# Kernel optimization log

Hardware: AMD Instinct MI355X
Metric: run time of the kernel (lower is better)

Reference implementation:

```python
import jax, jax.numpy as jnp
import numpy as np

WIN = 64
SHIFT = 32
HEADS = 12


def setup_inputs() -> dict:
    key = jax.random.key(0)
    ks = jax.random.split(key, 6)
    D = 768
    return {
        'x': jax.random.normal(ks[0], (16, 4096, D), dtype=jnp.float32),
        'qkv_w': jax.random.normal(ks[1], (3 * D, D), dtype=jnp.float32) * (D ** -0.5),
        'qkv_b': jax.random.normal(ks[2], (3 * D,), dtype=jnp.float32) * 0.02,
        'proj_w': jax.random.normal(ks[3], (D, D), dtype=jnp.float32) * (D ** -0.5),
        'proj_b': jax.random.normal(ks[4], (D,), dtype=jnp.float32) * 0.02,
        'rel_bias': jax.random.normal(ks[5], (HEADS, 2 * WIN - 1), dtype=jnp.float32) * 0.02,
    }


def reference(x, qkv_w, qkv_b, proj_w, proj_b, rel_bias):
    B, N, D = x.shape
    H, hd = HEADS, D // HEADS
    scale = hd ** -0.5
    if SHIFT:
        x = jnp.roll(x, SHIFT, axis=1)
    pad = (-N) % WIN
    if pad:
        x = jnp.pad(x, ((0, 0), (0, pad), (0, 0)))
    Np = x.shape[1]
    nW = Np // WIN
    # [B*nW, w, D] windows
    xw = x.reshape(B * nW, WIN, D)
    qkv = xw @ qkv_w.T + qkv_b                       # [B*nW, w, 3D]
    qkv = qkv.reshape(B * nW, WIN, 3, H, hd).transpose(2, 0, 3, 1, 4)
    q, k, v = qkv[0], qkv[1], qkv[2]                 # [B*nW, H, w, hd]
    attn = jnp.einsum('bhqd,bhkd->bhqk', q, k) * scale
    idx = jnp.arange(WIN)
    rel = idx[None, :] - idx[:, None] + (WIN - 1)    # [w, w] in [0, 2w-2]
    attn = attn + rel_bias[:, rel][None]             # gather bias per head
    attn = jax.nn.softmax(attn, axis=-1)
    y = jnp.einsum('bhqk,bhkd->bhqd', attn, v)       # [B*nW, H, w, hd]
    y = y.transpose(0, 2, 1, 3).reshape(B * nW, WIN, D)
    y = y @ proj_w.T + proj_b
    y = y.reshape(B, Np, D)
    if pad:
        y = y[:, :N, :]
    if SHIFT:
        y = jnp.roll(y, -SHIFT, axis=1)
    return y
```

## Files before the change

### kernel.cpp

```cpp
#include <hip/hip_runtime.h>
#include <hip/hip_bf16.h>
#include <stdint.h>

#define SEQ     4096
#define NBATCH  16
#define DMODEL  768
#define NHEAD   12
#define HDIM    64
#define WINSZ   64
#define SHIFT_T 32
#define QKV_N   (3*DMODEL)

typedef __attribute__((ext_vector_type(8))) short  bf16x8;
typedef __attribute__((ext_vector_type(4))) float  f32x4;

static __device__ __forceinline__ unsigned short f2bf(float f) {
  union { float f; unsigned u; } v; v.f = f;
  unsigned r = v.u + 0x7fffu + ((v.u >> 16) & 1u);
  return (unsigned short)(r >> 16);
}

#define G2L(gp, lp) __builtin_amdgcn_global_load_lds( \
    (const __attribute__((address_space(1))) unsigned*)(const void*)(gp), \
    (__attribute__((address_space(3))) unsigned*)(void*)(lp), 16, 0, 0)

__global__ void k_cvt_x(const float* __restrict__ x, unsigned short* __restrict__ xb,
                        long long c0, long long n8) {
  for (long long i = (long long)blockIdx.x*blockDim.x + threadIdx.x; i < n8;
       i += (long long)gridDim.x*blockDim.x) {
    long long e = i*8;
    int d = (int)(e % DMODEL);
    long long gt = c0 + e / DMODEL;
    int t = (int)(gt & (SEQ-1));
    long long b = gt >> 12;
    int ts = (t - SHIFT_T) & (SEQ-1);
    const float* src = x + (((b << 12) + ts) * (long long)DMODEL + d);
    float4 a0 = *(const float4*)src;
    float4 a1 = *(const float4*)(src + 4);
    bf16x8 o;
    o[0]=(short)f2bf(a0.x); o[1]=(short)f2bf(a0.y); o[2]=(short)f2bf(a0.z); o[3]=(short)f2bf(a0.w);
    o[4]=(short)f2bf(a1.x); o[5]=(short)f2bf(a1.y); o[6]=(short)f2bf(a1.z); o[7]=(short)f2bf(a1.w);
    *(bf16x8*)(xb + e) = o;
  }
}

__global__ void k_cvt_w(const float* __restrict__ w, unsigned short* __restrict__ wb, int n8) {
  int i = blockIdx.x*blockDim.x + threadIdx.x;
  if (i >= n8) return;
  float4 a0 = ((const float4*)w)[2*i];
  float4 a1 = ((const float4*)w)[2*i+1];
  bf16x8 o;
  o[0]=(short)f2bf(a0.x); o[1]=(short)f2bf(a0.y); o[2]=(short)f2bf(a0.z); o[3]=(short)f2bf(a0.w);
  o[4]=(short)f2bf(a1.x); o[5]=(short)f2bf(a1.y); o[6]=(short)f2bf(a1.z); o[7]=(short)f2bf(a1.w);
  ((bf16x8*)wb)[i] = o;
}

template<int MODE>
__global__ __launch_bounds__(512, 1)
void k_gemm256(const unsigned short* __restrict__ A, const unsigned short* __restrict__ Bw,
               const float* __restrict__ bias, unsigned short* __restrict__ Cb,
               float* __restrict__ Cf, int M, int N, int K, int nTN, long long c0) {
  __shared__ char lds[4*32768];
  const int nsl = K >> 5;
  int nwg = gridDim.x;
  int cpx = nwg >> 3;
  int wg  = (blockIdx.x & 7) * cpx + (blockIdx.x >> 3);
  int bm = wg / nTN, bn = wg - bm*nTN;
  long long m0 = (long long)bm * 256;
  int n0 = bn * 256;
  int tid = threadIdx.x;
  int lane = tid & 63, wid = tid >> 6;
  int wr = wid >> 2, wc = wid & 3;
  int cl = lane & 15, g4 = lane >> 4;

  const long long K2 = 2LL * K;
  int L  = tid * 16;
  int Ls = L ^ (((L >> 7) & 7) << 4);
  int srow = Ls >> 6;
  int scol = Ls & 63;
  const char* gA0 = (const char*)A + (m0 + srow) * K2 + scol;
  const char* gA1 = (const char*)A + (m0 + 128 + srow) * K2 + scol;
  const char* gB0 = (const char*)Bw + (long long)(n0 + srow) * K2 + scol;
  const char* gB1 = (const char*)Bw + (long long)(n0 + 128 + srow) * K2 + scol;
  int ldst = L;

  int aoff = (wr*8192 + cl*64 + g4*16) ^ ((cl >> 1) << 4);
  int boff = (16384 + wc*4096 + cl*64 + g4*16) ^ ((cl >> 1) << 4);

  f32x4 acc[8][4];
  #pragma unroll
  for (int i = 0; i < 8; ++i)
    #pragma unroll
    for (int j = 0; j < 4; ++j) acc[i][j] = (f32x4){0.f,0.f,0.f,0.f};

  {
    char* s0 = lds;
    char* s1 = lds + 32768;
    G2L(gA0,       s0 + ldst);
    G2L(gA1,       s0 + 8192  + ldst);
    G2L(gB0,       s0 + 16384 + ldst);
    G2L(gB1,       s0 + 24576 + ldst);
    G2L(gA0 + 64,  s1 + ldst);
    G2L(gA1 + 64,  s1 + 8192  + ldst);
    G2L(gB0 + 64,  s1 + 16384 + ldst);
    G2L(gB1 + 64,  s1 + 24576 + ldst);
    asm volatile("s_waitcnt vmcnt(4)" ::: "memory");
    __builtin_amdgcn_sched_barrier(0);
    __builtin_amdgcn_s_barrier();
  }

#define MFMA_ROW(av, m) \
    acc[m][0] = __builtin_amdgcn_mfma_f32_16x16x32_bf16(av, b0, acc[m][0], 0, 0, 0); \
    acc[m][1] = __builtin_amdgcn_mfma_f32_16x16x32_bf16(av, b1, acc[m][1], 0, 0, 0); \
    acc[m][2] = __builtin_amdgcn_mfma_f32_16x16x32_bf16(av, b2, acc[m][2], 0, 0, 0); \
    acc[m][3] = __builtin_amdgcn_mfma_f32_16x16x32_bf16(av, b3, acc[m][3], 0, 0, 0);

  for (int s = 0; s < nsl; ++s) {
    char* sb  = lds + ((s & 3) << 15);
    char* stb = lds + (((s + 2) & 3) << 15);
    long long kb2 = (long long)(s + 2) << 6;
    bool doStage = (s + 2) < nsl;

    bf16x8 a0 = *(const bf16x8*)(sb + aoff);
    bf16x8 a1 = *(const bf16x8*)(sb + aoff + 1024);
    bf16x8 a2 = *(const bf16x8*)(sb + aoff + 2048);
    bf16x8 a3 = *(const bf16x8*)(sb + aoff + 3072);
    bf16x8 b0 = *(const bf16x8*)(sb + boff);
    bf16x8 b1 = *(const bf16x8*)(sb + boff + 1024);
    bf16x8 b2 = *(const bf16x8*)(sb + boff + 2048);
    bf16x8 b3 = *(const bf16x8*)(sb + boff + 3072);
    if (doStage) {
      G2L(gA0 + kb2, stb + ldst);
      G2L(gA1 + kb2, stb + 8192 + ldst);
    }
    __builtin_amdgcn_sched_barrier(0);
    __builtin_amdgcn_s_barrier();
    asm volatile("s_waitcnt lgkmcnt(0)" ::: "memory");
    __builtin_amdgcn_sched_barrier(0);
    __builtin_amdgcn_s_setprio(1);
    MFMA_ROW(a0, 0)
    MFMA_ROW(a1, 1)
    MFMA_ROW(a2, 2)
    MFMA_ROW(a3, 3)
    __builtin_amdgcn_s_setprio(0);
    __builtin_amdgcn_sched_barrier(0);
    __builtin_amdgcn_s_barrier();

    bf16x8 a4 = *(const bf16x8*)(sb + aoff + 4096);
    bf16x8 a5 = *(const bf16x8*)(sb + aoff + 5120);
    bf16x8 a6 = *(const bf16x8*)(sb + aoff + 6144);
    bf16x8 a7 = *(const bf16x8*)(sb + aoff + 7168);
    if (doStage) {
      G2L(gB0 + kb2, stb + 16384 + ldst);
      G2L(gB1 + kb2, stb + 24576 + ldst);
      asm volatile("s_waitcnt vmcnt(4)" ::: "memory");
    } else if (s + 1 < nsl) {
      asm volatile("s_waitcnt vmcnt(0)" ::: "memory");
    }
    __builtin_amdgcn_sched_barrier(0);
    __builtin_amdgcn_s_barrier();
    asm volatile("s_waitcnt lgkmcnt(0)" ::: "memory");
    __builtin_amdgcn_sched_barrier(0);
    __builtin_amdgcn_s_setprio(1);
    MFMA_ROW(a4, 4)
    MFMA_ROW(a5, 5)
    MFMA_ROW(a6, 6)
    MFMA_ROW(a7, 7)
    __builtin_amdgcn_s_setprio(0);
    __builtin_amdgcn_sched_barrier(0);
    __builtin_amdgcn_s_barrier();
  }
#undef MFMA_ROW

  #pragma unroll
  for (int mf = 0; mf < 8; ++mf) {
    #pragma unroll
    for (int nf = 0; nf < 4; ++nf) {
      int n = n0 + wc*64 + nf*16 + cl;
      float bv = bias[n];
      #pragma unroll
      for (int r = 0; r < 4; ++r) {
        long long m = m0 + wr*128 + mf*16 + g4*4 + r;
        float v = acc[mf][nf][r] + bv;
        if (MODE == 0) {
          Cb[m * (long long)N + n] = f2bf(v);
        } else {
          long long gm = c0 + m;
          long long om = (gm & ~(long long)(SEQ-1)) | ((gm - SHIFT_T) & (long long)(SEQ-1));
          Cf[om * (long long)N + n] = v;
        }
      }
    }
  }
}

__global__ __launch_bounds__(256, 4)
void k_attn(const unsigned short* __restrict__ qkv, const float* __restrict__ rel_bias,
            unsigned short* __restrict__ y) {
  int w = blockIdx.x / NHEAD;
  int h = blockIdx.x - w*NHEAD;
  __shared__ unsigned short sQ[64*72], sK[64*72], sV[64*72];
  __shared__ unsigned short sP[4][16*72];
  __shared__ float rb[128];
  int tid = threadIdx.x, lane = tid & 63, wid = tid >> 6;
  int cl = lane & 15, g4 = lane >> 4;

  if (tid < 2*WINSZ - 1) rb[tid] = rel_bias[h*(2*WINSZ-1) + tid];

  const unsigned short* base = qkv + (long long)w*WINSZ*QKV_N + h*HDIM;
  #pragma unroll
  for (int pass = 0; pass < 2; ++pass) {
    int row = (tid >> 3) + pass*32;
    int ch  = tid & 7;
    const unsigned short* src = base + (long long)row*QKV_N + ch*8;
    *(bf16x8*)(sQ + row*72 + ch*8) = *(const bf16x8*)(src);
    *(bf16x8*)(sK + row*72 + ch*8) = *(const bf16x8*)(src + DMODEL);
    *(bf16x8*)(sV + row*72 + ch*8) = *(const bf16x8*)(src + 2*DMODEL);
  }
  __syncthreads();

  f32x4 sc[4];
  #pragma unroll
  for (int nt = 0; nt < 4; ++nt) sc[nt] = (f32x4){0.f,0.f,0.f,0.f};
  #pragma unroll
  for (int kk = 0; kk < 2; ++kk) {
    bf16x8 aq = *(const bf16x8*)(sQ + (wid*16 + cl)*72 + kk*32 + g4*8);
    #pragma unroll
    for (int nt = 0; nt < 4; ++nt) {
      bf16x8 bk = *(const bf16x8*)(sK + (nt*16 + cl)*72 + kk*32 + g4*8);
      sc[nt] = __builtin_amdgcn_mfma_f32_16x16x32_bf16(aq, bk, sc[nt], 0, 0, 0);
    }
  }

  float pv[4][4];
  #pragma unroll
  for (int r = 0; r < 4; ++r) {
    int qi = wid*16 + g4*4 + r;
    float mx = -1e30f;
    #pragma unroll
    for (int nt = 0; nt < 4; ++nt) {
      int kj = nt*16 + cl;
      float v = sc[nt][r]*0.125f + rb[kj - qi + (WINSZ-1)];
      pv[nt][r] = v;
      mx = fmaxf(mx, v);
    }
    #pragma unroll
    for (int m = 1; m < 16; m <<= 1) mx = fmaxf(mx, __shfl_xor(mx, m, 64));
    float sum = 0.f;
    #pragma unroll
    for (int nt = 0; nt < 4; ++nt) { float e = __expf(pv[nt][r]-mx); pv[nt][r] = e; sum += e; }
    #pragma unroll
    for (int m = 1; m < 16; m <<= 1) sum += __shfl_xor(sum, m, 64);
    float inv = 1.f / sum;
    #pragma unroll
    for (int nt = 0; nt < 4; ++nt)
      sP[wid][(g4*4+r)*72 + nt*16 + cl] = f2bf(pv[nt][r]*inv);
  }

  f32x4 o[4];
  #pragma unroll
  for (int nt = 0; nt < 4; ++nt) o[nt] = (f32x4){0.f,0.f,0.f,0.f};
  #pragma unroll
  for (int kk = 0; kk < 2; ++kk) {
    bf16x8 ap = *(const bf16x8*)(&sP[wid][cl*72 + kk*32 + g4*8]);
    #pragma unroll
    for (int nt = 0; nt < 4; ++nt) {
      bf16x8 bv;
      #pragma unroll
      for (int j = 0; j < 8; ++j)
        bv[j] = (short)sV[(kk*32 + g4*8 + j)*72 + nt*16 + cl];
      o[nt] = __builtin_amdgcn_mfma_f32_16x16x32_bf16(ap, bv, o[nt], 0, 0, 0);
    }
  }

  long long tokbase = (long long)w * WINSZ;
  #pragma unroll
  for (int nt = 0; nt < 4; ++nt)
    #pragma unroll
    for (int r = 0; r < 4; ++r) {
      int row = wid*16 + g4*4 + r;
      y[(tokbase + row) * (long long)DMODEL + h*HDIM + nt*16 + cl] = f2bf(o[nt][r]);
    }
}

extern "C" void kernel_launch(void* const* d_in, const int* in_sizes, int n_in,
                              void* d_out, int out_size, void* d_ws, size_t ws_size,
                              hipStream_t stream) {
  const float* x      = (const float*)d_in[0];
  const float* qkv_w  = (const float*)d_in[1];
  const float* qkv_b  = (const float*)d_in[2];
  const float* proj_w = (const float*)d_in[3];
  const float* proj_b = (const float*)d_in[4];
  const float* rel_b  = (const float*)d_in[5];
  float* out = (float*)d_out;

  const long long NTOK = (long long)NBATCH * SEQ;
  const size_t wbytes = (size_t)QKV_N*DMODEL*2 + (size_t)DMODEL*DMODEL*2;

  int C = 16;
  for (int c : {1, 2, 4, 8, 16}) {
    size_t tpc = (size_t)NTOK / c;
    size_t need = tpc*QKV_N*2 + tpc*DMODEL*2 + wbytes;
    if (need <= ws_size) { C = c; break; }
  }
  long long tpc = NTOK / C;

  char* ws = (char*)d_ws;
  unsigned short* qkvb = (unsigned short*)ws;
  unsigned short* xb   = (unsigned short*)(ws + (size_t)tpc*QKV_N*2);
  unsigned short* wq   = (unsigned short*)(ws + (size_t)tpc*QKV_N*2 + (size_t)tpc*DMODEL*2);
  unsigned short* wp   = wq + (size_t)QKV_N*DMODEL;

  k_cvt_w<<<(QKV_N*DMODEL/8 + 255)/256, 256, 0, stream>>>(qkv_w, wq, QKV_N*DMODEL/8);
  k_cvt_w<<<(DMODEL*DMODEL/8 + 255)/256, 256, 0, stream>>>(proj_w, wp, DMODEL*DMODEL/8);

  for (int c = 0; c < C; ++c) {
    long long c0 = (long long)c * tpc;
    long long n8 = tpc * DMODEL / 8;
    int cvtGrid = (int)((n8 + 255) / 256); if (cvtGrid > 2048) cvtGrid = 2048;
    k_cvt_x<<<cvtGrid, 256, 0, stream>>>(x, xb, c0, n8);

    int mT = (int)(tpc / 256);
    k_gemm256<0><<<mT * (QKV_N/256), 512, 0, stream>>>(xb, wq, qkv_b, qkvb, nullptr,
                                                       (int)tpc, QKV_N, DMODEL, QKV_N/256, c0);
    k_attn<<<(int)(tpc/WINSZ) * NHEAD, 256, 0, stream>>>(qkvb, rel_b, xb );
    k_gemm256<1><<<mT * (DMODEL/256), 512, 0, stream>>>(xb, wp, proj_b, nullptr, out,
                                                        (int)tpc, DMODEL, DMODEL, DMODEL/256, c0);
  }
}
```

Measured before the change: 525.7 us.

## Switch GEMM to 32x32x16 MFMA with single-phase unrolled K pipeline

Replaces the 16x16x32 MFMA tiling in the QKV/projection GEMM with 32x32x16 bf16 MFMAs. Each wave still covers a 128x64 tile, now as 4x2 32x32 blocks that need fewer LDS fragment loads per MFMA. The K loop becomes one phase per slice with both A and B staged together, manually unrolled by four ring slots, with fewer barriers per slice. The epilogue index mapping is updated for the 32x32 accumulator layout. This relies on nsl being at least 4, and on the four-slot ring with vmcnt(4) waits staying correct.

```diff
diff --git a/kernel.cpp b/kernel.cpp
--- a/kernel.cpp
+++ b/kernel.cpp
@@ -11,8 +11,9 @@
 #define SHIFT_T 32
 #define QKV_N   (3*DMODEL)
 
-typedef __attribute__((ext_vector_type(8))) short  bf16x8;
-typedef __attribute__((ext_vector_type(4))) float  f32x4;
+typedef __attribute__((ext_vector_type(8)))  short bf16x8;
+typedef __attribute__((ext_vector_type(4)))  float f32x4;
+typedef __attribute__((ext_vector_type(16))) float f32x16;
 
 static __device__ __forceinline__ unsigned short f2bf(float f) {
   union { float f; unsigned u; } v; v.f = f;
@@ -55,6 +56,8 @@
   ((bf16x8*)wb)[i] = o;
 }
 
+#define MFMA32(a,b,c) __builtin_amdgcn_mfma_f32_32x32x16_bf16(a,b,c,0,0,0)
+
 template<int MODE>
 __global__ __launch_bounds__(512, 1)
 void k_gemm256(const unsigned short* __restrict__ A, const unsigned short* __restrict__ Bw,
@@ -71,117 +74,106 @@
   int tid = threadIdx.x;
   int lane = tid & 63, wid = tid >> 6;
   int wr = wid >> 2, wc = wid & 3;
-  int cl = lane & 15, g4 = lane >> 4;
+  int l31 = lane & 31, h = lane >> 5;
 
   const long long K2 = 2LL * K;
   int L  = tid * 16;
   int Ls = L ^ (((L >> 7) & 7) << 4);
-  int srow = Ls >> 6;
-  int scol = Ls & 63;
+  int srow = Ls >> 6, scol = Ls & 63;
   const char* gA0 = (const char*)A + (m0 + srow) * K2 + scol;
   const char* gA1 = (const char*)A + (m0 + 128 + srow) * K2 + scol;
   const char* gB0 = (const char*)Bw + (long long)(n0 + srow) * K2 + scol;
   const char* gB1 = (const char*)Bw + (long long)(n0 + 128 + srow) * K2 + scol;
-  int ldst = L;
-
-  int aoff = (wr*8192 + cl*64 + g4*16) ^ ((cl >> 1) << 4);
-  int boff = (16384 + wc*4096 + cl*64 + g4*16) ^ ((cl >> 1) << 4);
-
-  f32x4 acc[8][4];
-  #pragma unroll
-  for (int i = 0; i < 8; ++i)
-    #pragma unroll
-    for (int j = 0; j < 4; ++j) acc[i][j] = (f32x4){0.f,0.f,0.f,0.f};
-
-  {
-    char* s0 = lds;
-    char* s1 = lds + 32768;
-    G2L(gA0,       s0 + ldst);
-    G2L(gA1,       s0 + 8192  + ldst);
-    G2L(gB0,       s0 + 16384 + ldst);
-    G2L(gB1,       s0 + 24576 + ldst);
-    G2L(gA0 + 64,  s1 + ldst);
-    G2L(gA1 + 64,  s1 + 8192  + ldst);
-    G2L(gB0 + 64,  s1 + 16384 + ldst);
-    G2L(gB1 + 64,  s1 + 24576 + ldst);
-    asm volatile("s_waitcnt vmcnt(4)" ::: "memory");
-    __builtin_amdgcn_sched_barrier(0);
-    __builtin_amdgcn_s_barrier();
-  }
-
-#define MFMA_ROW(av, m) \
-    acc[m][0] = __builtin_amdgcn_mfma_f32_16x16x32_bf16(av, b0, acc[m][0], 0, 0, 0); \
-    acc[m][1] = __builtin_amdgcn_mfma_f32_16x16x32_bf16(av, b1, acc[m][1], 0, 0, 0); \
-    acc[m][2] = __builtin_amdgcn_mfma_f32_16x16x32_bf16(av, b2, acc[m][2], 0, 0, 0); \
-    acc[m][3] = __builtin_amdgcn_mfma_f32_16x16x32_bf16(av, b3, acc[m][3], 0, 0, 0);
-
-  for (int s = 0; s < nsl; ++s) {
-    char* sb  = lds + ((s & 3) << 15);
-    char* stb = lds + (((s + 2) & 3) << 15);
-    long long kb2 = (long long)(s + 2) << 6;
-    bool doStage = (s + 2) < nsl;
-
-    bf16x8 a0 = *(const bf16x8*)(sb + aoff);
-    bf16x8 a1 = *(const bf16x8*)(sb + aoff + 1024);
-    bf16x8 a2 = *(const bf16x8*)(sb + aoff + 2048);
-    bf16x8 a3 = *(const bf16x8*)(sb + aoff + 3072);
-    bf16x8 b0 = *(const bf16x8*)(sb + boff);
-    bf16x8 b1 = *(const bf16x8*)(sb + boff + 1024);
-    bf16x8 b2 = *(const bf16x8*)(sb + boff + 2048);
-    bf16x8 b3 = *(const bf16x8*)(sb + boff + 3072);
-    if (doStage) {
-      G2L(gA0 + kb2, stb + ldst);
-      G2L(gA1 + kb2, stb + 8192 + ldst);
-    }
-    __builtin_amdgcn_sched_barrier(0);
-    __builtin_amdgcn_s_barrier();
-    asm volatile("s_waitcnt lgkmcnt(0)" ::: "memory");
-    __builtin_amdgcn_sched_barrier(0);
-    __builtin_amdgcn_s_setprio(1);
-    MFMA_ROW(a0, 0)
-    MFMA_ROW(a1, 1)
-    MFMA_ROW(a2, 2)
-    MFMA_ROW(a3, 3)
-    __builtin_amdgcn_s_setprio(0);
-    __builtin_amdgcn_sched_barrier(0);
-    __builtin_amdgcn_s_barrier();
-
-    bf16x8 a4 = *(const bf16x8*)(sb + aoff + 4096);
-    bf16x8 a5 = *(const bf16x8*)(sb + aoff + 5120);
-    bf16x8 a6 = *(const bf16x8*)(sb + aoff + 6144);
-    bf16x8 a7 = *(const bf16x8*)(sb + aoff + 7168);
-    if (doStage) {
-      G2L(gB0 + kb2, stb + 16384 + ldst);
-      G2L(gB1 + kb2, stb + 24576 + ldst);
-      asm volatile("s_waitcnt vmcnt(4)" ::: "memory");
-    } else if (s + 1 < nsl) {
-      asm volatile("s_waitcnt vmcnt(0)" ::: "memory");
-    }
-    __builtin_amdgcn_sched_barrier(0);
-    __builtin_amdgcn_s_barrier();
-    asm volatile("s_waitcnt lgkmcnt(0)" ::: "memory");
-    __builtin_amdgcn_sched_barrier(0);
-    __builtin_amdgcn_s_setprio(1);
-    MFMA_ROW(a4, 4)
-    MFMA_ROW(a5, 5)
-    MFMA_ROW(a6, 6)
-    MFMA_ROW(a7, 7)
-    __builtin_amdgcn_s_setprio(0);
-    __builtin_amdgcn_sched_barrier(0);
-    __builtin_amdgcn_s_barrier();
-  }
-#undef MFMA_ROW
-
-  #pragma unroll
-  for (int mf = 0; mf < 8; ++mf) {
-    #pragma unroll
-    for (int nf = 0; nf < 4; ++nf) {
-      int n = n0 + wc*64 + nf*16 + cl;
+
+  int axor  = ((l31 >> 1) & 7) << 4;
+  int aoff0 = wr*8192 + ((l31*64 + h*16) ^ axor);
+  int aoff1 = aoff0 ^ 32;
+  int boff0 = 16384 + (wc >> 1)*8192 + ((((wc & 1)*64 + l31)*64 + h*16) ^ axor);
+  int boff1 = boff0 ^ 32;
+
+  f32x16 acc[4][2];
+  #pragma unroll
+  for (int i = 0; i < 4; ++i)
+    #pragma unroll
+    for (int j = 0; j < 2; ++j)
+      #pragma unroll
+      for (int e = 0; e < 16; ++e) acc[i][j][e] = 0.f;
+
+  G2L(gA0,      lds + L);
+  G2L(gA1,      lds + 8192  + L);
+  G2L(gB0,      lds + 16384 + L);
+  G2L(gB1,      lds + 24576 + L);
+  G2L(gA0 + 64, lds + 32768 + L);
+  G2L(gA1 + 64, lds + 32768 + 8192  + L);
+  G2L(gB0 + 64, lds + 32768 + 16384 + L);
+  G2L(gB1 + 64, lds + 32768 + 24576 + L);
+  gA0 += 128; gA1 += 128; gB0 += 128; gB1 += 128;
+  asm volatile("s_waitcnt vmcnt(4)" ::: "memory");
+  __builtin_amdgcn_sched_barrier(0);
+  __builtin_amdgcn_s_barrier();
+
+#define SLICE(SLOT, STSLOT, DO_STAGE, VMASM) do {                          \
+    const char* sb = lds + (SLOT)*32768;                                   \
+    bf16x8 a0 = *(const bf16x8*)(sb + aoff0);                              \
+    bf16x8 a1 = *(const bf16x8*)(sb + aoff0 + 2048);                       \
+    bf16x8 a2 = *(const bf16x8*)(sb + aoff0 + 4096);                       \
+    bf16x8 a3 = *(const bf16x8*)(sb + aoff0 + 6144);                       \
+    bf16x8 a4 = *(const bf16x8*)(sb + aoff1);                              \
+    bf16x8 a5 = *(const bf16x8*)(sb + aoff1 + 2048);                       \
+    bf16x8 a6 = *(const bf16x8*)(sb + aoff1 + 4096);                       \
+    bf16x8 a7 = *(const bf16x8*)(sb + aoff1 + 6144);                       \
+    bf16x8 b0 = *(const bf16x8*)(sb + boff0);                              \
+    bf16x8 b1 = *(const bf16x8*)(sb + boff0 + 2048);                       \
+    bf16x8 b2 = *(const bf16x8*)(sb + boff1);                              \
+    bf16x8 b3 = *(const bf16x8*)(sb + boff1 + 2048);                       \
+    if (DO_STAGE) {                                                        \
+      char* st = lds + (STSLOT)*32768;                                     \
+      G2L(gA0, st + L);                                                    \
+      G2L(gA1, st + 8192  + L);                                            \
+      G2L(gB0, st + 16384 + L);                                            \
+      G2L(gB1, st + 24576 + L);                                            \
+    }                                                                      \
+    gA0 += 64; gA1 += 64; gB0 += 64; gB1 += 64;                            \
+    asm volatile(VMASM ::: "memory");                                      \
+    __builtin_amdgcn_sched_barrier(0);                                     \
+    __builtin_amdgcn_s_barrier();                                          \
+    __builtin_amdgcn_s_setprio(1);                                         \
+    acc[0][0]=MFMA32(a0,b0,acc[0][0]); acc[0][1]=MFMA32(a0,b1,acc[0][1]);  \
+    acc[1][0]=MFMA32(a1,b0,acc[1][0]); acc[1][1]=MFMA32(a1,b1,acc[1][1]);  \
+    acc[2][0]=MFMA32(a2,b0,acc[2][0]); acc[2][1]=MFMA32(a2,b1,acc[2][1]);  \
+    acc[3][0]=MFMA32(a3,b0,acc[3][0]); acc[3][1]=MFMA32(a3,b1,acc[3][1]);  \
+    acc[0][0]=MFMA32(a4,b2,acc[0][0]); acc[0][1]=MFMA32(a4,b3,acc[0][1]);  \
+    acc[1][0]=MFMA32(a5,b2,acc[1][0]); acc[1][1]=MFMA32(a5,b3,acc[1][1]);  \
+    acc[2][0]=MFMA32(a6,b2,acc[2][0]); acc[2][1]=MFMA32(a6,b3,acc[2][1]);  \
+    acc[3][0]=MFMA32(a7,b2,acc[3][0]); acc[3][1]=MFMA32(a7,b3,acc[3][1]);  \
+    __builtin_amdgcn_s_setprio(0);                                         \
+    __builtin_amdgcn_sched_barrier(0);                                     \
+    __builtin_amdgcn_s_barrier();                                          \
+  } while (0)
+
+  for (int os = 0; os + 8 <= nsl; os += 4) {
+    SLICE(0, 2, true, "s_waitcnt vmcnt(4)");
+    SLICE(1, 3, true, "s_waitcnt vmcnt(4)");
+    SLICE(2, 0, true, "s_waitcnt vmcnt(4)");
+    SLICE(3, 1, true, "s_waitcnt vmcnt(4)");
+  }
+  SLICE(0, 2, true,  "s_waitcnt vmcnt(4)");
+  SLICE(1, 3, true,  "s_waitcnt vmcnt(4)");
+  SLICE(2, 0, false, "s_waitcnt vmcnt(0)");
+  SLICE(3, 1, false, "");
+#undef SLICE
+
+  #pragma unroll
+  for (int mt = 0; mt < 4; ++mt) {
+    #pragma unroll
+    for (int nt = 0; nt < 2; ++nt) {
+      int n = n0 + wc*64 + nt*32 + l31;
       float bv = bias[n];
       #pragma unroll
-      for (int r = 0; r < 4; ++r) {
-        long long m = m0 + wr*128 + mf*16 + g4*4 + r;
-        float v = acc[mf][nf][r] + bv;
+      for (int reg = 0; reg < 16; ++reg) {
+        int rin = (reg & 3) + 8*(reg >> 2) + 4*h;
+        long long m = m0 + wr*128 + mt*32 + rin;
+        float v = acc[mt][nt][reg] + bv;
         if (MODE == 0) {
           Cb[m * (long long)N + n] = f2bf(v);
         } else {
```

New measurement: 545.9 us. +3.8%, slower.
